# Kernel tuning notes

Hardware: AMD Instinct MI355X
Metric: run time of the kernel (lower is better)

## Reference

```python
import jax, jax.numpy as jnp
import numpy as np
from jax.scipy.special import erf

N_POINTS = 5000
N_EVENTS = 1_000_000


def setup_inputs() -> dict:
    key = jax.random.key(0)
    k1, k2, k3, k4 = jax.random.split(key, 4)
    data_idx = jax.random.randint(k1, (N_EVENTS, 2), 0, N_POINTS, dtype=jnp.int32)
    data_t = jax.random.uniform(k2, (N_EVENTS,), dtype=jnp.float32) * 10.0
    # learned parameters, matching torch.rand(...)*0.5 init
    z0 = jax.random.uniform(k3, (N_POINTS, 2), dtype=jnp.float32) * 0.5
    v0 = jax.random.uniform(k4, (N_POINTS, 2), dtype=jnp.float32) * 0.5
    beta = jnp.ones((1, 1), dtype=jnp.float32)  # beta init = 1.0
    t0 = jnp.float32(0.0)
    tn = jnp.float32(10.0)
    return {"data_idx": data_idx, "data_t": data_t, "t0": t0, "tn": tn,
            "z0": z0, "v0": v0, "beta": beta}


def reference(data_idx, data_t, t0, tn, z0, v0, beta):
    b = beta[0, 0]
    # ---- event intensity: sum over events of (beta - ||z_i(t) - z_j(t)||^2)
    i = data_idx[:, 0]
    j = data_idx[:, 1]
    dz_e = (z0[i] - z0[j]) + (v0[i] - v0[j]) * data_t[:, None]  # [E,2]
    d_event = jnp.sum(dz_e * dz_e, axis=-1)                     # [E]
    n_events = data_t.shape[0]
    event_intensity = n_events * b - jnp.sum(d_event)

    # ---- non-event intensity: analytic integral over all node pairs i<j
    n = z0.shape[0]
    pi_idx, pj_idx = jnp.triu_indices(n, k=1)  # static node-pair list
    dz = z0[pi_idx] - z0[pj_idx]  # [P,2]
    dv = v0[pi_idx] - v0[pj_idx]  # [P,2]
    a2 = jnp.sum(dz * dz, axis=-1)       # ||dz||^2
    b2 = jnp.sum(dv * dv, axis=-1)       # ||dv||^2
    ab = jnp.sum(dz * dv, axis=-1)       # dz . dv
    bnorm = jnp.sqrt(b2)
    mu = ab / b2
    # integral_{t0}^{tn} exp(beta - ||dz + dv t||^2) dt
    #   = exp(beta - a2 + ab^2/b2) * sqrt(pi)/(2|dv|) * [erf(|dv|(tn+mu)) - erf(|dv|(t0+mu))]
    pref = jnp.exp(b - a2 + ab * mu) * (jnp.sqrt(jnp.pi) / (2.0 * bnorm))
    integral = pref * (erf(bnorm * (tn + mu)) - erf(bnorm * (t0 + mu)))
    non_event_intensity = jnp.sum(integral)

    log_likelihood = event_intensity - non_event_intensity
    return log_likelihood.reshape(1, 1)
```

## Files before the change

### kernel.cpp

```cpp
#include <hip/hip_runtime.h>
#include <math.h>

#define NTHR 256
#define MAXBLK 4096
#define PTS_PAD 20480


typedef float v2f __attribute__((ext_vector_type(2)));

__global__ void pack_kernel(const float* __restrict__ z0,
                            const float* __restrict__ v0,
                            float* __restrict__ xs, float* __restrict__ ys,
                            float* __restrict__ vxs, float* __restrict__ vys,
                            float4* __restrict__ pts, int n_pts) {
    int p = blockIdx.x * blockDim.x + threadIdx.x;
    if (p < n_pts) {
        float zx = z0[2 * p], zy = z0[2 * p + 1];
        float vx = v0[2 * p], vy = v0[2 * p + 1];
        xs[p] = zx; ys[p] = zy; vxs[p] = vx; vys[p] = vy;
        pts[p] = make_float4(zx, zy, vx, vy);
    }
}

#define ERF_A1 0.0705230784f
#define ERF_A2 0.0422820123f
#define ERF_A3 0.0092705272f
#define ERF_A4 0.0001520143f
#define ERF_A5 0.0002765672f
#define ERF_A6 0.0000430638f

__device__ __forceinline__ float erf728(float x) {
    float ax = fabsf(x);
    float h = fmaf(ERF_A6, ax, ERF_A5);
    h = fmaf(h, ax, ERF_A4);
    h = fmaf(h, ax, ERF_A3);
    h = fmaf(h, ax, ERF_A2);
    h = fmaf(h, ax, ERF_A1);
    float u = fmaf(h, ax, 1.0f);
    float w = __builtin_amdgcn_rcpf(u);
    w = w * w; w = w * w; w = w * w; w = w * w;
    return copysignf(1.0f - w, x);
}

__device__ __forceinline__ float pair_val(float4 Pi, float4 Pj,
                                          float b, float t0, float tn) {
    const float SPI2 = 0.88622692545275801365f;
    const float L2E  = 1.4426950408889634f;
    float dzx = Pi.x - Pj.x, dzy = Pi.y - Pj.y;
    float dvx = Pi.z - Pj.z, dvy = Pi.w - Pj.w;
    float a2 = fmaf(dzx, dzx, dzy * dzy);
    float b2 = fmaf(dvx, dvx, dvy * dvy);
    float ab = fmaf(dzx, dvx, dzy * dvy);
    float r  = __builtin_amdgcn_rsqf(b2);
    float mu = ab * (r * r);
    float e0 = fmaf(ab, mu, b - a2);
    float E  = __builtin_amdgcn_exp2f(e0 * L2E);
    float bn = b2 * r;
    float x1 = bn * (tn + mu);
    float x0 = bn * (t0 + mu);
    return (E * (SPI2 * r)) * (erf728(x1) - erf728(x0));
}

__device__ __forceinline__ v2f erf_u2(v2f ax) {
    v2f h = ERF_A6 * ax + ERF_A5;
    h = h * ax + ERF_A4;
    h = h * ax + ERF_A3;
    h = h * ax + ERF_A2;
    h = h * ax + ERF_A1;
    return h * ax + 1.0f;
}

__device__ __forceinline__ v2f pair_val2(float Pix, float Piy, float Pivx,
                                         float Pivy, v2f xj, v2f yj, v2f vxj,
                                         v2f vyj, float b, float t0, float tn) {
    const float SPI2 = 0.88622692545275801365f;
    const float L2E  = 1.4426950408889634f;
    v2f dzx = Pix - xj, dzy = Piy - yj;
    v2f dvx = Pivx - vxj, dvy = Pivy - vyj;
    v2f a2 = dzx * dzx + dzy * dzy;
    v2f b2 = dvx * dvx + dvy * dvy;
    v2f ab = dzx * dvx + dzy * dvy;
    v2f r;  r.x = __builtin_amdgcn_rsqf(b2.x); r.y = __builtin_amdgcn_rsqf(b2.y);
    v2f mu = ab * (r * r);
    v2f e0 = ab * mu + (b - a2);
    v2f E;  E.x = __builtin_amdgcn_exp2f(e0.x * L2E);
            E.y = __builtin_amdgcn_exp2f(e0.y * L2E);
    v2f bn = b2 * r;
    v2f x1 = bn * (tn + mu);
    v2f x0 = bn * (t0 + mu);
    v2f ax1; ax1.x = fabsf(x1.x); ax1.y = fabsf(x1.y);
    v2f ax0; ax0.x = fabsf(x0.x); ax0.y = fabsf(x0.y);
    v2f u1 = erf_u2(ax1);
    v2f u0 = erf_u2(ax0);
    v2f p = u1 * u0;
    v2f rp; rp.x = __builtin_amdgcn_rcpf(p.x); rp.y = __builtin_amdgcn_rcpf(p.y);
    v2f w1 = u0 * rp;
    v2f w0 = u1 * rp;
    w1 = w1 * w1; w1 = w1 * w1; w1 = w1 * w1; w1 = w1 * w1;
    w0 = w0 * w0; w0 = w0 * w0; w0 = w0 * w0; w0 = w0 * w0;
    v2f e1 = 1.0f - w1;
    v2f e0f = 1.0f - w0;
    e1.x = copysignf(e1.x, x1.x);  e1.y = copysignf(e1.y, x1.y);
    e0f.x = copysignf(e0f.x, x0.x); e0f.y = copysignf(e0f.y, x0.y);
    return (E * (r * SPI2)) * (e1 - e0f);
}

__device__ __forceinline__ float row_sweep(const float* __restrict__ xs,
                                           const float* __restrict__ ys,
                                           const float* __restrict__ vxs,
                                           const float* __restrict__ vys,
                                           const float4* __restrict__ pts,
                                           int r, int n_pts,
                                           float b, float t0, float tn) {
    float4 Pi = pts[r];
    float head = 0.0f;
    int base = r + 1;
    if (base & 1) {
        if (threadIdx.x == 0)
            head = pair_val(Pi, pts[base], b, t0, tn);
        ++base;
    }
    v2f acc = {0.f, 0.f};
    for (int jb = base + 2 * (int)threadIdx.x; jb < n_pts; jb += 2 * NTHR) {
        v2f xj  = *(const v2f*)(xs + jb);
        v2f yj  = *(const v2f*)(ys + jb);
        v2f vxj = *(const v2f*)(vxs + jb);
        v2f vyj = *(const v2f*)(vys + jb);
        acc += pair_val2(Pi.x, Pi.y, Pi.z, Pi.w, xj, yj, vxj, vyj, b, t0, tn);
    }
    return head + acc.x + acc.y;
}

__device__ __forceinline__ float event_sum(const int2* __restrict__ idx,
                                           const float* __restrict__ t,
                                           const float4* __restrict__ pts,
                                           int n_events, int nblocks) {
    const int4*   idx4 = (const int4*)idx;
    const float2* t2   = (const float2*)t;
    const int half = n_events >> 1;
    float acc = 0.0f;
    for (int h = blockIdx.x * NTHR + threadIdx.x; h < half;
         h += nblocks * NTHR) {
        int4 ij = idx4[h];
        float2 tt = t2[h];
        float4 pi0 = pts[ij.x], pj0 = pts[ij.y];
        float4 pi1 = pts[ij.z], pj1 = pts[ij.w];
        float dx0 = (pi0.x - pj0.x) + (pi0.z - pj0.z) * tt.x;
        float dy0 = (pi0.y - pj0.y) + (pi0.w - pj0.w) * tt.x;
        float dx1 = (pi1.x - pj1.x) + (pi1.z - pj1.z) * tt.y;
        float dy1 = (pi1.y - pj1.y) + (pi1.w - pj1.w) * tt.y;
        acc = fmaf(dx0, dx0, fmaf(dy0, dy0, acc));
        acc = fmaf(dx1, dx1, fmaf(dy1, dy1, acc));
    }
    if ((n_events & 1) && blockIdx.x == 0 && threadIdx.x == 0) {
        int e = n_events - 1;
        int2 ij = idx[e];
        float te = t[e];
        float4 pi = pts[ij.x], pj = pts[ij.y];
        float dx = (pi.x - pj.x) + (pi.z - pj.z) * te;
        float dy = (pi.y - pj.y) + (pi.w - pj.w) * te;
        acc = fmaf(dx, dx, fmaf(dy, dy, acc));
    }
    return acc;
}

__device__ __forceinline__ float pair_sum(const float* __restrict__ xs,
                                          const float* __restrict__ ys,
                                          const float* __restrict__ vxs,
                                          const float* __restrict__ vys,
                                          const float4* __restrict__ pts,
                                          int n_pts, float b, float t0,
                                          float tn) {
    const int n_rows = n_pts - 1;
    const int r1 = blockIdx.x;
    float acc = 0.0f;
    if (r1 < n_rows) {
        const int r2 = n_rows - 1 - r1;
        acc += row_sweep(xs, ys, vxs, vys, pts, r1, n_pts, b, t0, tn);
        if (r2 > r1)
            acc += row_sweep(xs, ys, vxs, vys, pts, r2, n_pts, b, t0, tn);
    }
    return acc;
}

__global__ __launch_bounds__(NTHR) void cvm_main_kernel(
    const int2* __restrict__ idx, const float* __restrict__ t,
    const float* __restrict__ xs, const float* __restrict__ ys,
    const float* __restrict__ vxs, const float* __restrict__ vys,
    const float4* __restrict__ pts,
    const float* __restrict__ t0p, const float* __restrict__ tnp,
    const float* __restrict__ betap,
    int n_events, int n_pts, double* __restrict__ partials) {

    const float b  = betap[0];
    const float t0 = t0p[0];
    const float tn = tnp[0];
    const int nblocks = gridDim.x;

    float accf;
    if ((threadIdx.x >> 6) & 1) {
        accf = pair_sum(xs, ys, vxs, vys, pts, n_pts, b, t0, tn);
        accf += event_sum(idx, t, pts, n_events, nblocks);
    } else {
        accf = event_sum(idx, t, pts, n_events, nblocks);
        accf += pair_sum(xs, ys, vxs, vys, pts, n_pts, b, t0, tn);
    }

    double v = (double)accf;
    #pragma unroll
    for (int off = 32; off > 0; off >>= 1) v += __shfl_down(v, off, 64);
    __shared__ double wsum[4];
    if ((threadIdx.x & 63) == 0) wsum[threadIdx.x >> 6] = v;
    __syncthreads();
    if (threadIdx.x == 0)
        partials[blockIdx.x] = wsum[0] + wsum[1] + wsum[2] + wsum[3];
}

__global__ void finish_kernel(const double* __restrict__ partials, int nblk,
                              const float* __restrict__ betap,
                              float* __restrict__ out, int n_events) {
    double v = 0.0;
    for (int i = threadIdx.x; i < nblk; i += NTHR) v += partials[i];
    #pragma unroll
    for (int off = 32; off > 0; off >>= 1) v += __shfl_down(v, off, 64);
    __shared__ double wsum[4];
    if ((threadIdx.x & 63) == 0) wsum[threadIdx.x >> 6] = v;
    __syncthreads();
    if (threadIdx.x == 0)
        out[0] = (float)((double)n_events * (double)betap[0] -
                         (wsum[0] + wsum[1] + wsum[2] + wsum[3]));
}

extern "C" void kernel_launch(void* const* d_in, const int* in_sizes, int n_in,
                              void* d_out, int out_size, void* d_ws, size_t ws_size,
                              hipStream_t stream) {
    const int2*  idx  = (const int2*)d_in[0];
    const float* t    = (const float*)d_in[1];
    const float* t0   = (const float*)d_in[2];
    const float* tn   = (const float*)d_in[3];
    const float* z0   = (const float*)d_in[4];
    const float* v0   = (const float*)d_in[5];
    const float* beta = (const float*)d_in[6];
    const int n_events = in_sizes[1];
    const int n_pts    = in_sizes[4] / 2;

    char* base = (char*)d_ws;
    double* partials = (double*)base;
    float* xs  = (float*)(base + 32768);
    float* ys  = (float*)(base + 32768 + PTS_PAD);
    float* vxs = (float*)(base + 32768 + 2 * PTS_PAD);
    float* vys = (float*)(base + 32768 + 3 * PTS_PAD);
    float4* pts = (float4*)(base + 32768 + 4 * PTS_PAD);

    const int n_rows = n_pts - 1;
    int nblk = (n_rows + 1) / 2;
    if (nblk < 1) nblk = 1;
    if (nblk > MAXBLK) nblk = MAXBLK;

    pack_kernel<<<(n_pts + NTHR - 1) / NTHR, NTHR, 0, stream>>>(
        z0, v0, xs, ys, vxs, vys, pts, n_pts);
    cvm_main_kernel<<<nblk, NTHR, 0, stream>>>(idx, t, xs, ys, vxs, vys, pts,
                                               t0, tn, beta, n_events, n_pts,
                                               partials);
    finish_kernel<<<1, NTHR, 0, stream>>>(partials, nblk, beta,
                                          (float*)d_out, n_events);
}
```

Baseline: 96.60 us.

## Use cheaper 4-term erf approximation, simplify pair algebra, fuse final reduction

Replaces the 6-coefficient erf approximation (16th-power) with the Abramowitz-Stegun 7.1.27 form (4 coefficients, 4th power), reducing per-pair ALU work at reduced accuracy. It rewrites mu-based terms using c = ab*rsqrt(b2), saving multiplies. It also removes the separate finish kernel by having the last block, detected with an atomic counter reset in the pack kernel, sum the partials. This saves one launch but the erf error grows to about 5e-4.

```diff
diff --git a/kernel.cpp b/kernel.cpp
--- a/kernel.cpp
+++ b/kernel.cpp
@@ -12,7 +12,8 @@
                             const float* __restrict__ v0,
                             float* __restrict__ xs, float* __restrict__ ys,
                             float* __restrict__ vxs, float* __restrict__ vys,
-                            float4* __restrict__ pts, int n_pts) {
+                            float4* __restrict__ pts,
+                            unsigned int* __restrict__ counter, int n_pts) {
     int p = blockIdx.x * blockDim.x + threadIdx.x;
     if (p < n_pts) {
         float zx = z0[2 * p], zy = z0[2 * p + 1];
@@ -20,25 +21,22 @@
         xs[p] = zx; ys[p] = zy; vxs[p] = vx; vys[p] = vy;
         pts[p] = make_float4(zx, zy, vx, vy);
     }
-}
-
-#define ERF_A1 0.0705230784f
-#define ERF_A2 0.0422820123f
-#define ERF_A3 0.0092705272f
-#define ERF_A4 0.0001520143f
-#define ERF_A5 0.0002765672f
-#define ERF_A6 0.0000430638f
-
-__device__ __forceinline__ float erf728(float x) {
+    if (p == 0) *counter = 0u;
+}
+
+#define E27_A1 0.278393f
+#define E27_A2 0.230389f
+#define E27_A3 0.000972f
+#define E27_A4 0.078108f
+
+__device__ __forceinline__ float erf727(float x) {
     float ax = fabsf(x);
-    float h = fmaf(ERF_A6, ax, ERF_A5);
-    h = fmaf(h, ax, ERF_A4);
-    h = fmaf(h, ax, ERF_A3);
-    h = fmaf(h, ax, ERF_A2);
-    h = fmaf(h, ax, ERF_A1);
+    float h = fmaf(E27_A4, ax, E27_A3);
+    h = fmaf(h, ax, E27_A2);
+    h = fmaf(h, ax, E27_A1);
     float u = fmaf(h, ax, 1.0f);
     float w = __builtin_amdgcn_rcpf(u);
-    w = w * w; w = w * w; w = w * w; w = w * w;
+    w = w * w; w = w * w;
     return copysignf(1.0f - w, x);
 }
 
@@ -52,21 +50,19 @@
     float b2 = fmaf(dvx, dvx, dvy * dvy);
     float ab = fmaf(dzx, dvx, dzy * dvy);
     float r  = __builtin_amdgcn_rsqf(b2);
-    float mu = ab * (r * r);
-    float e0 = fmaf(ab, mu, b - a2);
+    float c  = ab * r;
+    float e0 = fmaf(c, c, b - a2);
     float E  = __builtin_amdgcn_exp2f(e0 * L2E);
     float bn = b2 * r;
-    float x1 = bn * (tn + mu);
-    float x0 = bn * (t0 + mu);
-    return (E * (SPI2 * r)) * (erf728(x1) - erf728(x0));
-}
-
-__device__ __forceinline__ v2f erf_u2(v2f ax) {
-    v2f h = ERF_A6 * ax + ERF_A5;
-    h = h * ax + ERF_A4;
-    h = h * ax + ERF_A3;
-    h = h * ax + ERF_A2;
-    h = h * ax + ERF_A1;
+    float x1 = fmaf(bn, tn, c);
+    float x0 = fmaf(bn, t0, c);
+    return (E * (SPI2 * r)) * (erf727(x1) - erf727(x0));
+}
+
+__device__ __forceinline__ v2f erf_u27(v2f ax) {
+    v2f h = E27_A4 * ax + E27_A3;
+    h = h * ax + E27_A2;
+    h = h * ax + E27_A1;
     return h * ax + 1.0f;
 }
 
@@ -81,23 +77,23 @@
     v2f b2 = dvx * dvx + dvy * dvy;
     v2f ab = dzx * dvx + dzy * dvy;
     v2f r;  r.x = __builtin_amdgcn_rsqf(b2.x); r.y = __builtin_amdgcn_rsqf(b2.y);
-    v2f mu = ab * (r * r);
-    v2f e0 = ab * mu + (b - a2);
+    v2f c  = ab * r;
+    v2f e0 = c * c + (b - a2);
     v2f E;  E.x = __builtin_amdgcn_exp2f(e0.x * L2E);
             E.y = __builtin_amdgcn_exp2f(e0.y * L2E);
     v2f bn = b2 * r;
-    v2f x1 = bn * (tn + mu);
-    v2f x0 = bn * (t0 + mu);
+    v2f x1 = bn * tn + c;
+    v2f x0 = bn * t0 + c;
     v2f ax1; ax1.x = fabsf(x1.x); ax1.y = fabsf(x1.y);
     v2f ax0; ax0.x = fabsf(x0.x); ax0.y = fabsf(x0.y);
-    v2f u1 = erf_u2(ax1);
-    v2f u0 = erf_u2(ax0);
+    v2f u1 = erf_u27(ax1);
+    v2f u0 = erf_u27(ax0);
     v2f p = u1 * u0;
     v2f rp; rp.x = __builtin_amdgcn_rcpf(p.x); rp.y = __builtin_amdgcn_rcpf(p.y);
     v2f w1 = u0 * rp;
     v2f w0 = u1 * rp;
-    w1 = w1 * w1; w1 = w1 * w1; w1 = w1 * w1; w1 = w1 * w1;
-    w0 = w0 * w0; w0 = w0 * w0; w0 = w0 * w0; w0 = w0 * w0;
+    w1 = w1 * w1; w1 = w1 * w1;
+    w0 = w0 * w0; w0 = w0 * w0;
     v2f e1 = 1.0f - w1;
     v2f e0f = 1.0f - w0;
     e1.x = copysignf(e1.x, x1.x);  e1.y = copysignf(e1.y, x1.y);
@@ -190,7 +186,9 @@
     const float4* __restrict__ pts,
     const float* __restrict__ t0p, const float* __restrict__ tnp,
     const float* __restrict__ betap,
-    int n_events, int n_pts, double* __restrict__ partials) {
+    int n_events, int n_pts,
+    double* __restrict__ partials, unsigned int* __restrict__ counter,
+    float* __restrict__ out) {
 
     const float b  = betap[0];
     const float t0 = t0p[0];
@@ -210,25 +208,28 @@
     #pragma unroll
     for (int off = 32; off > 0; off >>= 1) v += __shfl_down(v, off, 64);
     __shared__ double wsum[4];
+    __shared__ bool is_last;
     if ((threadIdx.x & 63) == 0) wsum[threadIdx.x >> 6] = v;
     __syncthreads();
-    if (threadIdx.x == 0)
+    if (threadIdx.x == 0) {
         partials[blockIdx.x] = wsum[0] + wsum[1] + wsum[2] + wsum[3];
-}
-
-__global__ void finish_kernel(const double* __restrict__ partials, int nblk,
-                              const float* __restrict__ betap,
-                              float* __restrict__ out, int n_events) {
-    double v = 0.0;
-    for (int i = threadIdx.x; i < nblk; i += NTHR) v += partials[i];
-    #pragma unroll
-    for (int off = 32; off > 0; off >>= 1) v += __shfl_down(v, off, 64);
-    __shared__ double wsum[4];
-    if ((threadIdx.x & 63) == 0) wsum[threadIdx.x >> 6] = v;
+        __threadfence();
+        unsigned int old = atomicAdd(counter, 1u);
+        is_last = (old == (unsigned int)(nblocks - 1));
+    }
     __syncthreads();
-    if (threadIdx.x == 0)
-        out[0] = (float)((double)n_events * (double)betap[0] -
-                         (wsum[0] + wsum[1] + wsum[2] + wsum[3]));
+    if (is_last) {
+        __threadfence();
+        double s = 0.0;
+        for (int i = threadIdx.x; i < nblocks; i += NTHR) s += partials[i];
+        #pragma unroll
+        for (int off = 32; off > 0; off >>= 1) s += __shfl_down(s, off, 64);
+        if ((threadIdx.x & 63) == 0) wsum[threadIdx.x >> 6] = s;
+        __syncthreads();
+        if (threadIdx.x == 0)
+            out[0] = (float)((double)n_events * (double)betap[0] -
+                             (wsum[0] + wsum[1] + wsum[2] + wsum[3]));
+    }
 }
 
 extern "C" void kernel_launch(void* const* d_in, const int* in_sizes, int n_in,
@@ -246,6 +247,7 @@
 
     char* base = (char*)d_ws;
     double* partials = (double*)base;
+    unsigned int* counter = (unsigned int*)(base + MAXBLK * sizeof(double));
     float* xs  = (float*)(base + 32768);
     float* ys  = (float*)(base + 32768 + PTS_PAD);
     float* vxs = (float*)(base + 32768 + 2 * PTS_PAD);
@@ -258,10 +260,8 @@
     if (nblk > MAXBLK) nblk = MAXBLK;
 
     pack_kernel<<<(n_pts + NTHR - 1) / NTHR, NTHR, 0, stream>>>(
-        z0, v0, xs, ys, vxs, vys, pts, n_pts);
+        z0, v0, xs, ys, vxs, vys, pts, counter, n_pts);
     cvm_main_kernel<<<nblk, NTHR, 0, stream>>>(idx, t, xs, ys, vxs, vys, pts,
                                                t0, tn, beta, n_events, n_pts,
-                                               partials);
-    finish_kernel<<<1, NTHR, 0, stream>>>(partials, nblk, beta,
-                                          (float*)d_out, n_events);
-}
+                                               partials, counter, (float*)d_out);
+}
```

Measured after the change: 143.6 us. 48.6% more time.
